# Kernel optimization log

Measured on AMD Instinct MI355X. Metric: run time of the kernel, lower is better.

## Reference

```python
import jax, jax.numpy as jnp
import numpy as np

B = 262144
NUM_CLASSES = 1000
ALPHA = 1.0  # init arg


def setup_inputs() -> dict:
    key = jax.random.key(0)
    k1, k2, k3 = jax.random.split(key, 3)
    output = jax.random.normal(k1, (B, 4 + NUM_CLASSES), dtype=jnp.float32)
    # target: [xmin, ymin, xmax, ymax, class_id] with valid integer class ids
    boxes = jax.random.uniform(k2, (B, 4), dtype=jnp.float32)
    class_ids = jax.random.randint(k3, (B, 1), 0, NUM_CLASSES).astype(jnp.float32)
    target = jnp.concatenate([boxes, class_ids], axis=1)
    return {"output": output, "target": target}


def reference(output, target):
    # ---- localization loss (vectorized over batch) ----
    box_pred = output[:, 0:4]  # [B,4] = (cx, cy, w, h)
    xmin, ymin, xmax, ymax = target[:, 0], target[:, 1], target[:, 2], target[:, 3]
    box_true = jnp.stack(
        [(xmin + xmax) * 0.5, (ymin + ymax) * 0.5, xmax - xmin, ymax - ymin],
        axis=1,
    )  # [B,4] = (cx, cy, w, h)
    loc_loss = jnp.mean((box_pred - box_true) ** 2, axis=1)  # [B], mse over 4 elems

    # ---- classification loss: cross entropy per sample ----
    logits = output[:, 4:]  # [B, C]
    class_ids = target[:, 4].astype(jnp.int32)  # [B]
    logp = jax.nn.log_softmax(logits, axis=-1)  # [B, C]
    class_loss = -jnp.take_along_axis(logp, class_ids[:, None], axis=1)[:, 0]  # [B]

    return jnp.mean(loc_loss + ALPHA * class_loss)
```

## Files before the change

### kernel.cpp

```cpp
#include <hip/hip_runtime.h>
#include <math.h>


#define ROWLEN 1004
#define NVEC   250

__global__ __launch_bounds__(256) void loc_loss_kernel(
    const float* __restrict__ output,
    const float* __restrict__ target,
    float* __restrict__ out,
    int n_rows, float inv_n)
{
    const int lane          = threadIdx.x & 63;
    const int wave_in_block = threadIdx.x >> 6;
    const int wave_id       = blockIdx.x * 4 + wave_in_block;
    const int num_waves     = gridDim.x * 4;

    float acc = 0.0f;

    for (int row = wave_id; row < n_rows; row += num_waves) {
        const float* rb = output + (size_t)row * ROWLEN;

        float t0 = 0.f, t1 = 0.f, t2 = 0.f, t3 = 0.f;
        float bp0 = 0.f, bp1 = 0.f, bp2 = 0.f, bp3 = 0.f;
        float logit_c = 0.f;
        if (lane == 0) {
            const float* tr = target + (size_t)row * 5;
            t0 = tr[0]; t1 = tr[1]; t2 = tr[2]; t3 = tr[3];
            int cls = (int)tr[4];
            logit_c = rb[4 + cls];
            bp0 = rb[0]; bp1 = rb[1]; bp2 = rb[2]; bp3 = rb[3];
        }

        const float4* lb = (const float4*)(rb + 4);
        float4 v0 = lb[lane];
        float4 v1 = lb[lane + 64];
        float4 v2 = lb[lane + 128];
        float4 v3;
        if (lane < NVEC - 192) {
            v3 = lb[lane + 192];
        } else {
            v3.x = -INFINITY; v3.y = -INFINITY; v3.z = -INFINITY; v3.w = -INFINITY;
        }

        float m = fmaxf(fmaxf(fmaxf(v0.x, v0.y), fmaxf(v0.z, v0.w)),
                        fmaxf(fmaxf(v1.x, v1.y), fmaxf(v1.z, v1.w)));
        m = fmaxf(m, fmaxf(fmaxf(v2.x, v2.y), fmaxf(v2.z, v2.w)));
        m = fmaxf(m, fmaxf(fmaxf(v3.x, v3.y), fmaxf(v3.z, v3.w)));

        float s = __expf(v0.x - m) + __expf(v0.y - m) + __expf(v0.z - m) + __expf(v0.w - m);
        s += __expf(v1.x - m) + __expf(v1.y - m) + __expf(v1.z - m) + __expf(v1.w - m);
        s += __expf(v2.x - m) + __expf(v2.y - m) + __expf(v2.z - m) + __expf(v2.w - m);
        s += __expf(v3.x - m) + __expf(v3.y - m) + __expf(v3.z - m) + __expf(v3.w - m);

        #pragma unroll
        for (int off = 1; off < 64; off <<= 1) {
            float mo = __shfl_xor(m, off, 64);
            float so = __shfl_xor(s, off, 64);
            float M  = fmaxf(m, mo);
            s = s * __expf(m - M) + so * __expf(mo - M);
            m = M;
        }

        if (lane == 0) {
            float lse = m + __logf(s);
            float cx = (t0 + t2) * 0.5f;
            float cy = (t1 + t3) * 0.5f;
            float w  = t2 - t0;
            float h  = t3 - t1;
            float dx = bp0 - cx, dy = bp1 - cy, dw = bp2 - w, dh = bp3 - h;
            float loc = (dx * dx + dy * dy + dw * dw + dh * dh) * 0.25f;
            acc += loc + (lse - logit_c);
        }
    }

    __shared__ float part[4];
    if (lane == 0) part[wave_in_block] = acc;
    __syncthreads();
    if (threadIdx.x == 0) {
        float tot = (part[0] + part[1] + part[2] + part[3]) * inv_n;
        atomicAdd(out, tot);
    }
}

extern "C" void kernel_launch(void* const* d_in, const int* in_sizes, int n_in,
                              void* d_out, int out_size, void* d_ws, size_t ws_size,
                              hipStream_t stream) {
    const float* output = (const float*)d_in[0];
    const float* target = (const float*)d_in[1];
    float* out = (float*)d_out;

    int n_rows = in_sizes[0] / ROWLEN;
    float inv_n = 1.0f / (float)n_rows;

    hipMemsetAsync(out, 0, out_size * sizeof(float), stream);

    loc_loss_kernel<<<4096, 256, 0, stream>>>(output, target, out, n_rows, inv_n);
}
```

Baseline: 1.294 ms.

## Process two rows per wave with two-pass max/sum and shuffle-based target logit

Each wave now handles two rows per iteration, issuing both rows' loads together to raise memory-level parallelism. The online max/sum shuffle merge is replaced by a separate max reduction followed by a sum reduction, which removes the per-step exp calls. The target logit is taken from registers with a lane shuffle instead of a separate global load by lane 0. This raises register pressure and adds a second reduction pass.

```diff
diff --git a/kernel.cpp b/kernel.cpp
--- a/kernel.cpp
+++ b/kernel.cpp
@@ -4,6 +4,10 @@
 
 #define ROWLEN 1004
 #define NVEC   250
+#define TAIL   58
+
+#define ESUM4(v, m) (__expf((v).x - (m)) + __expf((v).y - (m)) + \
+                     __expf((v).z - (m)) + __expf((v).w - (m)))
 
 __global__ __launch_bounds__(256) void loc_loss_kernel(
     const float* __restrict__ output,
@@ -18,59 +22,93 @@
 
     float acc = 0.0f;
 
-    for (int row = wave_id; row < n_rows; row += num_waves) {
-        const float* rb = output + (size_t)row * ROWLEN;
+    for (int rowA = wave_id; rowA < n_rows; rowA += 2 * num_waves) {
+        const int  rowB  = rowA + num_waves;
+        const bool hasB  = rowB < n_rows;
+        const int  rowB_ = hasB ? rowB : rowA;
 
-        float t0 = 0.f, t1 = 0.f, t2 = 0.f, t3 = 0.f;
-        float bp0 = 0.f, bp1 = 0.f, bp2 = 0.f, bp3 = 0.f;
-        float logit_c = 0.f;
-        if (lane == 0) {
-            const float* tr = target + (size_t)row * 5;
-            t0 = tr[0]; t1 = tr[1]; t2 = tr[2]; t3 = tr[3];
-            int cls = (int)tr[4];
-            logit_c = rb[4 + cls];
-            bp0 = rb[0]; bp1 = rb[1]; bp2 = rb[2]; bp3 = rb[3];
+        const float* rbA = output + (size_t)rowA  * ROWLEN;
+        const float* rbB = output + (size_t)rowB_ * ROWLEN;
+        const float* trA = target + (size_t)rowA  * 5;
+        const float* trB = target + (size_t)rowB_ * 5;
+
+        const float4* lbA = (const float4*)(rbA + 4);
+        const float4* lbB = (const float4*)(rbB + 4);
+
+        float4 a0 = lbA[lane];
+        float4 b0 = lbB[lane];
+        float4 a1 = lbA[lane + 64];
+        float4 b1 = lbB[lane + 64];
+        float4 a2 = lbA[lane + 128];
+        float4 b2 = lbB[lane + 128];
+        float4 a3, b3;
+        if (lane < TAIL) {
+            a3 = lbA[lane + 192];
+            b3 = lbB[lane + 192];
+        } else {
+            a3.x = a3.y = a3.z = a3.w = -INFINITY;
+            b3.x = b3.y = b3.z = b3.w = -INFINITY;
         }
 
-        const float4* lb = (const float4*)(rb + 4);
-        float4 v0 = lb[lane];
-        float4 v1 = lb[lane + 64];
-        float4 v2 = lb[lane + 128];
-        float4 v3;
-        if (lane < NVEC - 192) {
-            v3 = lb[lane + 192];
-        } else {
-            v3.x = -INFINITY; v3.y = -INFINITY; v3.z = -INFINITY; v3.w = -INFINITY;
-        }
+        float4 bpA = *(const float4*)rbA;
+        float4 bpB = *(const float4*)rbB;
+        float a_t0 = trA[0], a_t1 = trA[1], a_t2 = trA[2], a_t3 = trA[3];
+        int   a_cls = (int)trA[4];
+        float b_t0 = trB[0], b_t1 = trB[1], b_t2 = trB[2], b_t3 = trB[3];
+        int   b_cls = (int)trB[4];
 
-        float m = fmaxf(fmaxf(fmaxf(v0.x, v0.y), fmaxf(v0.z, v0.w)),
-                        fmaxf(fmaxf(v1.x, v1.y), fmaxf(v1.z, v1.w)));
-        m = fmaxf(m, fmaxf(fmaxf(v2.x, v2.y), fmaxf(v2.z, v2.w)));
-        m = fmaxf(m, fmaxf(fmaxf(v3.x, v3.y), fmaxf(v3.z, v3.w)));
-
-        float s = __expf(v0.x - m) + __expf(v0.y - m) + __expf(v0.z - m) + __expf(v0.w - m);
-        s += __expf(v1.x - m) + __expf(v1.y - m) + __expf(v1.z - m) + __expf(v1.w - m);
-        s += __expf(v2.x - m) + __expf(v2.y - m) + __expf(v2.z - m) + __expf(v2.w - m);
-        s += __expf(v3.x - m) + __expf(v3.y - m) + __expf(v3.z - m) + __expf(v3.w - m);
+        float mA = fmaxf(fmaxf(fmaxf(a0.x, a0.y), fmaxf(a0.z, a0.w)),
+                         fmaxf(fmaxf(a1.x, a1.y), fmaxf(a1.z, a1.w)));
+        float mB = fmaxf(fmaxf(fmaxf(b0.x, b0.y), fmaxf(b0.z, b0.w)),
+                         fmaxf(fmaxf(b1.x, b1.y), fmaxf(b1.z, b1.w)));
+        mA = fmaxf(mA, fmaxf(fmaxf(a2.x, a2.y), fmaxf(a2.z, a2.w)));
+        mB = fmaxf(mB, fmaxf(fmaxf(b2.x, b2.y), fmaxf(b2.z, b2.w)));
+        mA = fmaxf(mA, fmaxf(fmaxf(a3.x, a3.y), fmaxf(a3.z, a3.w)));
+        mB = fmaxf(mB, fmaxf(fmaxf(b3.x, b3.y), fmaxf(b3.z, b3.w)));
 
         #pragma unroll
         for (int off = 1; off < 64; off <<= 1) {
-            float mo = __shfl_xor(m, off, 64);
-            float so = __shfl_xor(s, off, 64);
-            float M  = fmaxf(m, mo);
-            s = s * __expf(m - M) + so * __expf(mo - M);
-            m = M;
+            mA = fmaxf(mA, __shfl_xor(mA, off, 64));
+            mB = fmaxf(mB, __shfl_xor(mB, off, 64));
+        }
+
+        int avi = a_cls >> 2, ac = a_cls & 3, asrc = avi & 63, aj = avi >> 6;
+        int bvi = b_cls >> 2, bc = b_cls & 3, bsrc = bvi & 63, bj = bvi >> 6;
+        float4 avj = (aj == 0) ? a0 : (aj == 1) ? a1 : (aj == 2) ? a2 : a3;
+        float4 bvj = (bj == 0) ? b0 : (bj == 1) ? b1 : (bj == 2) ? b2 : b3;
+        float acand = (ac == 0) ? avj.x : (ac == 1) ? avj.y : (ac == 2) ? avj.z : avj.w;
+        float bcand = (bc == 0) ? bvj.x : (bc == 1) ? bvj.y : (bc == 2) ? bvj.z : bvj.w;
+        float a_logit = __shfl(acand, asrc, 64);
+        float b_logit = __shfl(bcand, bsrc, 64);
+
+        float sA = ESUM4(a0, mA) + ESUM4(a1, mA) + ESUM4(a2, mA) + ESUM4(a3, mA);
+        float sB = ESUM4(b0, mB) + ESUM4(b1, mB) + ESUM4(b2, mB) + ESUM4(b3, mB);
+
+        #pragma unroll
+        for (int off = 1; off < 64; off <<= 1) {
+            sA += __shfl_xor(sA, off, 64);
+            sB += __shfl_xor(sB, off, 64);
         }
 
         if (lane == 0) {
-            float lse = m + __logf(s);
-            float cx = (t0 + t2) * 0.5f;
-            float cy = (t1 + t3) * 0.5f;
-            float w  = t2 - t0;
-            float h  = t3 - t1;
-            float dx = bp0 - cx, dy = bp1 - cy, dw = bp2 - w, dh = bp3 - h;
-            float loc = (dx * dx + dy * dy + dw * dw + dh * dh) * 0.25f;
-            acc += loc + (lse - logit_c);
+            {
+                float lse = mA + __logf(sA);
+                float cx = (a_t0 + a_t2) * 0.5f;
+                float cy = (a_t1 + a_t3) * 0.5f;
+                float w  = a_t2 - a_t0;
+                float h  = a_t3 - a_t1;
+                float dx = bpA.x - cx, dy = bpA.y - cy, dw = bpA.z - w, dh = bpA.w - h;
+                acc += (dx * dx + dy * dy + dw * dw + dh * dh) * 0.25f + (lse - a_logit);
+            }
+            if (hasB) {
+                float lse = mB + __logf(sB);
+                float cx = (b_t0 + b_t2) * 0.5f;
+                float cy = (b_t1 + b_t3) * 0.5f;
+                float w  = b_t2 - b_t0;
+                float h  = b_t3 - b_t1;
+                float dx = bpB.x - cx, dy = bpB.y - cy, dw = bpB.z - w, dh = bpB.w - h;
+                acc += (dx * dx + dy * dy + dw * dw + dh * dh) * 0.25f + (lse - b_logit);
+            }
         }
     }
 
```

New measurement: 1.297 ms. About the same (+0.2%).
